# Kernel tuning notes

Measured on AMD Instinct MI355X. Metric: run time of the kernel, lower is better.

Reference implementation:

```python
import jax, jax.numpy as jnp
import numpy as np

NU, NI, DU, DI, E, B, T = 100000, 50000, 256, 256, 128, 8192, 24

def setup_inputs() -> dict:
    key = jax.random.key(0)
    ks = jax.random.split(key, 12)
    s = 0.05
    return {
        "nodes": jax.random.randint(ks[0], (B,), 0, NU),
        "neigh_idx": jax.random.randint(ks[1], (B, T), 0, NI),
        "u_weight": jax.random.normal(ks[2], (NU, DU), jnp.float32),
        "i_weight": jax.random.normal(ks[3], (NI, DI), jnp.float32),
        "uW": jax.random.normal(ks[4], (DU, E), jnp.float32) * s,
        "ub": jnp.zeros((E,), jnp.float32),
        "iW": jax.random.normal(ks[5], (DI, E), jnp.float32) * s,
        "ib": jnp.zeros((E,), jnp.float32),
        "aW1": jax.random.normal(ks[6], (2 * E, E), jnp.float32) * s,
        "ab1": jnp.zeros((E,), jnp.float32),
        "aW2": jax.random.normal(ks[7], (E, E), jnp.float32) * s,
        "ab2": jnp.zeros((E,), jnp.float32),
        "aW3": jax.random.normal(ks[8], (E, 1), jnp.float32) * s,
        "ab3": jnp.zeros((1,), jnp.float32),
    }


def reference(nodes, neigh_idx, u_weight, i_weight, uW, ub, iW, ib,
              aW1, ab1, aW2, ab2, aW3, ab3):
    # node features: u_layer(ufeature.weight[nodes])  -> [B, E]
    nodes_fea = u_weight[nodes] @ uW + ub
    # neighbor features: i_layer(ifeature.weight[interactions]) -> [B, T, E]
    neighs = i_weight[neigh_idx] @ iW + ib
    # attention MLP over cat(neigh_feat, node_feat.repeat) -> softmax over T
    x = jnp.concatenate(
        [neighs, jnp.broadcast_to(nodes_fea[:, None, :], neighs.shape)], axis=-1)
    h = jax.nn.relu(x @ aW1 + ab1)
    h = jax.nn.relu(h @ aW2 + ab2)
    logits = (h @ aW3 + ab3)[..., 0]            # [B, T]
    att = jax.nn.softmax(logits, axis=-1)       # softmax over neighbors (dim=0 per node)
    # attention-weighted aggregation: neighs_feature.T @ att_w  -> [B, E]
    agg = jnp.einsum('bt,bte->be', att, neighs)
    # scatter into embed_matrix rows of the batch nodes
    embed_matrix = jnp.zeros((NU, E), jnp.float32).at[nodes].set(agg)
    return nodes_fea, embed_matrix
```

## Files before the change

kernel.cpp:

```cpp
#include <hip/hip_runtime.h>
#include <math.h>

#define NU 100000
#define NI 50000
#define DK 256
#define EN 128
#define BB 8192
#define TT 24

typedef short short8 __attribute__((ext_vector_type(8)));
typedef float f32x4  __attribute__((ext_vector_type(4)));

#define WPACK_SHORTS 114688
#define WP_OFF     0
#define OWNER_OFF  229376
#define NTAB_OFF   629376
#define NPART_OFF  13429376

#define OFF_IWT   0
#define OFF_UWT   32768
#define OFF_AW1UT 65536
#define OFF_AW1LT 81920
#define OFF_AW2T  98304

#define NBLK_NEIGH 782
#define NBLK_NF    128
#define NBLK_PACK  448
#define ATTN_BLKS  (BB / 2)

__device__ __forceinline__ unsigned short f2b(float x) {
    unsigned int u = __float_as_uint(x);
    u = (u + 0x7FFFu + ((u >> 16) & 1u)) >> 16;
    return (unsigned short)u;
}
__device__ __forceinline__ float b2f(unsigned short v) {
    return __uint_as_float(((unsigned int)v) << 16);
}

#define MFMA(a, b, c) __builtin_amdgcn_mfma_f32_16x16x32_bf16((a), (b), (c), 0, 0, 0)
#define LDROW(buf, stride, row, k) \
    (*reinterpret_cast<const short8*>(reinterpret_cast<const char*>(buf) + (row) * (stride) + (k) * 2))

__global__ __launch_bounds__(256)
void prep_kernel(const int* __restrict__ nodes,
                 const float* __restrict__ uW, const float* __restrict__ iW,
                 const float* __restrict__ aW1, const float* __restrict__ aW2,
                 short* __restrict__ wp, int* __restrict__ owner)
{
    if (blockIdx.x < NBLK_PACK) {
        int i = blockIdx.x * 256 + threadIdx.x;
        float v;
        if (i < 32768)      { int j = i;         int n = j >> 8, k = j & 255; v = iW[k * EN + n]; }
        else if (i < 65536) { int j = i - 32768; int n = j >> 8, k = j & 255; v = uW[k * EN + n]; }
        else if (i < 81920) { int j = i - 65536; int n = j >> 7, k = j & 127; v = aW1[k * EN + n]; }
        else if (i < 98304) { int j = i - 81920; int n = j >> 7, k = j & 127; v = aW1[(128 + k) * EN + n]; }
        else                { int j = i - 98304; int n = j >> 7, k = j & 127; v = aW2[k * EN + n]; }
        wp[i] = (short)f2b(v);
    } else {
        int b = (blockIdx.x - NBLK_PACK) * 256 + threadIdx.x;
        if (b < BB) owner[nodes[b]] = -1;
    }
}

__global__ __launch_bounds__(256, 4)
void embed_kernel(const int* __restrict__ nodes,
                  const float* __restrict__ u_weight, const float* __restrict__ i_weight,
                  const float* __restrict__ ub, const float* __restrict__ ib,
                  const float* __restrict__ ab1,
                  const short* __restrict__ wp, int* __restrict__ owner,
                  short* __restrict__ ntab, float* __restrict__ out_nf,
                  float* __restrict__ npart)
{
    __shared__ __align__(16) char smem[33792];
    __shared__ int sNd[64];

    const int tid = threadIdx.x;
    const int l = tid & 63, lr = l & 15, lq = l >> 4, n0 = (tid >> 6) * 32;
    const int kA = lq * 8, nc0 = n0 + lr, nc1 = n0 + 16 + lr;

    if (blockIdx.x < NBLK_NEIGH) {
        const int r0 = blockIdx.x * 64;
        const int nrows = (NI - r0 < 64) ? (NI - r0) : 64;

        for (int task = tid; task < 64 * 32; task += 256) {
            int row = task >> 5, c = task & 31;
            if (row < nrows) {
                const float* src = i_weight + (size_t)(r0 + row) * DK + c * 8;
                float4 f0 = *(const float4*)src;
                float4 f1 = *(const float4*)(src + 4);
                short8 o;
                o[0]=f2b(f0.x); o[1]=f2b(f0.y); o[2]=f2b(f0.z); o[3]=f2b(f0.w);
                o[4]=f2b(f1.x); o[5]=f2b(f1.y); o[6]=f2b(f1.z); o[7]=f2b(f1.w);
                *reinterpret_cast<short8*>(smem + row * 528 + c * 16) = o;
            }
        }
        __syncthreads();

        const short* iWt = wp + OFF_IWT;
        f32x4 acc[4][2];
        #pragma unroll
        for (int m = 0; m < 4; ++m) { acc[m][0] = {0.f,0.f,0.f,0.f}; acc[m][1] = {0.f,0.f,0.f,0.f}; }
        #pragma unroll
        for (int ks = 0; ks < 8; ++ks) {
            int k = ks * 32 + kA;
            short8 w0 = *reinterpret_cast<const short8*>(iWt + nc0 * DK + k);
            short8 w1 = *reinterpret_cast<const short8*>(iWt + nc1 * DK + k);
            #pragma unroll
            for (int m = 0; m < 4; ++m) {
                short8 a = LDROW(smem, 528, m * 16 + lr, k);
                acc[m][0] = MFMA(a, w0, acc[m][0]);
                acc[m][1] = MFMA(a, w1, acc[m][1]);
            }
        }
        __syncthreads();
        {
            float ib0 = ib[nc0], ib1 = ib[nc1];
            #pragma unroll
            for (int m = 0; m < 4; ++m)
                #pragma unroll
                for (int nt = 0; nt < 2; ++nt) {
                    int n = nt ? nc1 : nc0;
                    float bv = nt ? ib1 : ib0;
                    #pragma unroll
                    for (int r = 0; r < 4; ++r) {
                        int row = m * 16 + lq * 4 + r;
                        *reinterpret_cast<short*>(smem + row * 264 + n * 2)
                            = (short)f2b(acc[m][nt][r] + bv);
                    }
                }
        }
        __syncthreads();
        for (int g = tid; g < nrows * 16; g += 256) {
            int row = g >> 4, s = g & 15;
            short8 v = *reinterpret_cast<const short8*>(smem + row * 264 + s * 16);
            *reinterpret_cast<short8*>(ntab + (size_t)(r0 + row) * EN + s * 8) = v;
        }
    } else {
        const int bblk = blockIdx.x - NBLK_NEIGH;
        const int r0 = bblk * 64;
        {
            int bq = bblk * 256 + tid;
            if (bq < BB) atomicMax(&owner[nodes[bq]], bq);
        }
        if (tid < 64) sNd[tid] = nodes[r0 + tid];
        __syncthreads();

        for (int task = tid; task < 64 * 32; task += 256) {
            int row = task >> 5, c = task & 31;
            const float* src = u_weight + (size_t)sNd[row] * DK + c * 8;
            float4 f0 = *(const float4*)src;
            float4 f1 = *(const float4*)(src + 4);
            short8 o;
            o[0]=f2b(f0.x); o[1]=f2b(f0.y); o[2]=f2b(f0.z); o[3]=f2b(f0.w);
            o[4]=f2b(f1.x); o[5]=f2b(f1.y); o[6]=f2b(f1.z); o[7]=f2b(f1.w);
            *reinterpret_cast<short8*>(smem + row * 528 + c * 16) = o;
        }
        __syncthreads();

        const short* uWt   = wp + OFF_UWT;
        const short* aW1Lt = wp + OFF_AW1LT;

        f32x4 acc[4][2];
        #pragma unroll
        for (int m = 0; m < 4; ++m) { acc[m][0] = {0.f,0.f,0.f,0.f}; acc[m][1] = {0.f,0.f,0.f,0.f}; }
        #pragma unroll
        for (int ks = 0; ks < 8; ++ks) {
            int k = ks * 32 + kA;
            short8 w0 = *reinterpret_cast<const short8*>(uWt + nc0 * DK + k);
            short8 w1 = *reinterpret_cast<const short8*>(uWt + nc1 * DK + k);
            #pragma unroll
            for (int m = 0; m < 4; ++m) {
                short8 a = LDROW(smem, 528, m * 16 + lr, k);
                acc[m][0] = MFMA(a, w0, acc[m][0]);
                acc[m][1] = MFMA(a, w1, acc[m][1]);
            }
        }
        __syncthreads();
        {
            float b0v = ub[nc0], b1v = ub[nc1];
            #pragma unroll
            for (int m = 0; m < 4; ++m)
                #pragma unroll
                for (int nt = 0; nt < 2; ++nt) {
                    int n = nt ? nc1 : nc0;
                    float bv = nt ? b1v : b0v;
                    #pragma unroll
                    for (int r = 0; r < 4; ++r) {
                        int row = m * 16 + lq * 4 + r;
                        float v = acc[m][nt][r] + bv;
                        out_nf[(size_t)(r0 + row) * EN + n] = v;
                        *reinterpret_cast<short*>(smem + row * 272 + n * 2) = (short)f2b(v);
                    }
                }
        }
        __syncthreads();

        f32x4 ap[4][2];
        #pragma unroll
        for (int m = 0; m < 4; ++m) { ap[m][0] = {0.f,0.f,0.f,0.f}; ap[m][1] = {0.f,0.f,0.f,0.f}; }
        #pragma unroll
        for (int ks = 0; ks < 4; ++ks) {
            int k = ks * 32 + kA;
            short8 w0 = *reinterpret_cast<const short8*>(aW1Lt + nc0 * EN + k);
            short8 w1 = *reinterpret_cast<const short8*>(aW1Lt + nc1 * EN + k);
            #pragma unroll
            for (int m = 0; m < 4; ++m) {
                short8 a = LDROW(smem, 272, m * 16 + lr, k);
                ap[m][0] = MFMA(a, w0, ap[m][0]);
                ap[m][1] = MFMA(a, w1, ap[m][1]);
            }
        }
        {
            float b0v = ab1[nc0], b1v = ab1[nc1];
            #pragma unroll
            for (int m = 0; m < 4; ++m)
                #pragma unroll
                for (int nt = 0; nt < 2; ++nt) {
                    int n = nt ? nc1 : nc0;
                    float bv = nt ? b1v : b0v;
                    #pragma unroll
                    for (int r = 0; r < 4; ++r) {
                        int row = m * 16 + lq * 4 + r;
                        npart[(size_t)(r0 + row) * EN + n] = ap[m][nt][r] + bv;
                    }
                }
        }
    }
}

__global__ __launch_bounds__(256, 4)
void attn_kernel(const int* __restrict__ nodes, const int* __restrict__ neigh_idx,
                 const float* __restrict__ ab2, const float* __restrict__ aW3,
                 const float* __restrict__ ab3, const short* __restrict__ wp,
                 const short* __restrict__ ntab, const float* __restrict__ npart,
                 const int* __restrict__ owner, float* __restrict__ out_embed)
{
    __shared__ __align__(16) short sNg[48 * 136];
    __shared__ __align__(16) short sH1[48 * 136];
    __shared__ float sNp[256];
    __shared__ float sLogP[4][48];
    __shared__ float sAtt[48];

    const int tid = threadIdx.x;
    const int b0  = blockIdx.x * 2;

    const int node0 = nodes[b0], node1 = nodes[b0 + 1];
    const int own0  = owner[node0], own1 = owner[node1];

    sNp[tid] = npart[(size_t)b0 * EN + tid];

    for (int task = tid; task < 48 * 16; task += 256) {
        int row = task >> 4, s = task & 15;
        int idx = neigh_idx[b0 * TT + row];
        short8 v = *reinterpret_cast<const short8*>(ntab + (size_t)idx * EN + s * 8);
        *reinterpret_cast<short8*>(reinterpret_cast<char*>(sNg) + row * 272 + s * 16) = v;
    }
    __syncthreads();

    const int l = tid & 63, lr = l & 15, lq = l >> 4;
    const int wid = tid >> 6, n0 = wid * 32;
    const int kA = lq * 8, nc0 = n0 + lr, nc1 = n0 + 16 + lr;
    const short* aW1Ut = wp + OFF_AW1UT;
    const short* aW2t  = wp + OFF_AW2T;

    f32x4 a1[3][2];
    #pragma unroll
    for (int m = 0; m < 3; ++m) { a1[m][0] = {0.f,0.f,0.f,0.f}; a1[m][1] = {0.f,0.f,0.f,0.f}; }
    #pragma unroll
    for (int ks = 0; ks < 4; ++ks) {
        int k = ks * 32 + kA;
        short8 w0 = *reinterpret_cast<const short8*>(aW1Ut + nc0 * EN + k);
        short8 w1 = *reinterpret_cast<const short8*>(aW1Ut + nc1 * EN + k);
        #pragma unroll
        for (int m = 0; m < 3; ++m) {
            short8 a = LDROW(sNg, 272, m * 16 + lr, k);
            a1[m][0] = MFMA(a, w0, a1[m][0]);
            a1[m][1] = MFMA(a, w1, a1[m][1]);
        }
    }
    #pragma unroll
    for (int m = 0; m < 3; ++m)
        #pragma unroll
        for (int nt = 0; nt < 2; ++nt) {
            int n = nt ? nc1 : nc0;
            #pragma unroll
            for (int r = 0; r < 4; ++r) {
                int row = m * 16 + lq * 4 + r;
                int g = (row >= TT) ? 1 : 0;
                float v = fmaxf(a1[m][nt][r] + sNp[g * EN + n], 0.f);
                *reinterpret_cast<short*>(reinterpret_cast<char*>(sH1) + row * 272 + n * 2)
                    = (short)f2b(v);
            }
        }
    __syncthreads();

    f32x4 a2[3][2];
    #pragma unroll
    for (int m = 0; m < 3; ++m) { a2[m][0] = {0.f,0.f,0.f,0.f}; a2[m][1] = {0.f,0.f,0.f,0.f}; }
    #pragma unroll
    for (int ks = 0; ks < 4; ++ks) {
        int k = ks * 32 + kA;
        short8 w0 = *reinterpret_cast<const short8*>(aW2t + nc0 * EN + k);
        short8 w1 = *reinterpret_cast<const short8*>(aW2t + nc1 * EN + k);
        #pragma unroll
        for (int m = 0; m < 3; ++m) {
            short8 a = LDROW(sH1, 272, m * 16 + lr, k);
            a2[m][0] = MFMA(a, w0, a2[m][0]);
            a2[m][1] = MFMA(a, w1, a2[m][1]);
        }
    }
    {
        float b0v = ab2[nc0], b1v = ab2[nc1];
        float w3a = aW3[nc0], w3b = aW3[nc1];
        #pragma unroll
        for (int m = 0; m < 3; ++m) {
            float lp[4];
            #pragma unroll
            for (int r = 0; r < 4; ++r) {
                float v0 = fmaxf(a2[m][0][r] + b0v, 0.f);
                float v1 = fmaxf(a2[m][1][r] + b1v, 0.f);
                lp[r] = v0 * w3a + v1 * w3b;
            }
            #pragma unroll
            for (int r = 0; r < 4; ++r) {
                float v = lp[r];
                v += __shfl_xor(v, 1, 16);
                v += __shfl_xor(v, 2, 16);
                v += __shfl_xor(v, 4, 16);
                v += __shfl_xor(v, 8, 16);
                if (lr == 0) sLogP[wid][m * 16 + lq * 4 + r] = v;
            }
        }
    }
    __syncthreads();

    if (tid < 64) {
        float s48 = 0.f;
        if (tid < 48)
            s48 = sLogP[0][tid] + sLogP[1][tid] + sLogP[2][tid] + sLogP[3][tid] + ab3[0];
        int g = tid >> 5, tt = tid & 31;
        float v = __shfl(s48, g * 24 + tt, 64);
        v = (tt < TT) ? v : -1e30f;
        float mx = v;
        #pragma unroll
        for (int d = 16; d > 0; d >>= 1) mx = fmaxf(mx, __shfl_xor(mx, d, 32));
        float p = (tt < TT) ? __expf(v - mx) : 0.f;
        float s = p;
        #pragma unroll
        for (int d = 16; d > 0; d >>= 1) s += __shfl_xor(s, d, 32);
        if (tt < TT) sAtt[g * TT + tt] = p / s;
    }
    __syncthreads();

    {
        int g = tid >> 7, e = tid & 127;
        float a = 0.f;
        #pragma unroll
        for (int t = 0; t < TT; ++t) {
            unsigned short nv = *reinterpret_cast<const unsigned short*>(
                reinterpret_cast<const char*>(sNg) + (g * TT + t) * 272 + e * 2);
            a += sAtt[g * TT + t] * b2f(nv);
        }
        int node = g ? node1 : node0;
        int own  = g ? own1  : own0;
        if (own == b0 + g)
            out_embed[(size_t)node * EN + e] = a;
    }

    {
        float4* embed4 = (float4*)out_embed;
        const int n16 = NU * EN / 4;
        const int gsz = ATTN_BLKS * 256;
        float4 z = {0.f, 0.f, 0.f, 0.f};
        for (int i = blockIdx.x * 256 + tid; i < n16; i += gsz) {
            if (owner[i >> 5] < 0) embed4[i] = z;
        }
    }
}

extern "C" void kernel_launch(void* const* d_in, const int* in_sizes, int n_in,
                              void* d_out, int out_size, void* d_ws, size_t ws_size,
                              hipStream_t stream) {
    const int*   nodes     = (const int*)d_in[0];
    const int*   neigh_idx = (const int*)d_in[1];
    const float* u_weight  = (const float*)d_in[2];
    const float* i_weight  = (const float*)d_in[3];
    const float* uW  = (const float*)d_in[4];
    const float* ub  = (const float*)d_in[5];
    const float* iW  = (const float*)d_in[6];
    const float* ib  = (const float*)d_in[7];
    const float* aW1 = (const float*)d_in[8];
    const float* ab1 = (const float*)d_in[9];
    const float* aW2 = (const float*)d_in[10];
    const float* ab2 = (const float*)d_in[11];
    const float* aW3 = (const float*)d_in[12];
    const float* ab3 = (const float*)d_in[13];

    float* out_nf    = (float*)d_out;
    float* out_embed = out_nf + (size_t)BB * EN;

    char*  ws    = (char*)d_ws;
    short* wpack = (short*)(ws + WP_OFF);
    int*   owner = (int*)(ws + OWNER_OFF);
    short* ntab  = (short*)(ws + NTAB_OFF);
    float* npart = (float*)(ws + NPART_OFF);

    prep_kernel<<<NBLK_PACK + 32, 256, 0, stream>>>(nodes, uW, iW, aW1, aW2, wpack, owner);
    embed_kernel<<<NBLK_NEIGH + NBLK_NF, 256, 0, stream>>>(
        nodes, u_weight, i_weight, ub, ib, ab1, wpack, owner, ntab, out_nf, npart);
    attn_kernel<<<ATTN_BLKS, 256, 0, stream>>>(nodes, neigh_idx, ab2, aW3, ab3,
                                               wpack, ntab, npart, owner, out_embed);
}
```

Before: 87.72 us.

## Process four nodes per attention block and move embed zero-fill into embed kernel

```diff
diff --git a/kernel.cpp b/kernel.cpp
--- a/kernel.cpp
+++ b/kernel.cpp
@@ -26,7 +26,8 @@
 #define NBLK_NEIGH 782
 #define NBLK_NF    128
 #define NBLK_PACK  448
-#define ATTN_BLKS  (BB / 2)
+#define GGA 4
+#define ATTN_BLKS  (BB / GGA)
 
 __device__ __forceinline__ unsigned short f2b(float x) {
     unsigned int u = __float_as_uint(x);
@@ -35,6 +36,11 @@
 }
 __device__ __forceinline__ float b2f(unsigned short v) {
     return __uint_as_float(((unsigned int)v) << 16);
+}
+__device__ __forceinline__ unsigned int cvtpk_bf16(float lo, float hi) {
+    unsigned int r;
+    asm("v_cvt_pk_bf16_f32 %0, %1, %2" : "=v"(r) : "v"(lo), "v"(hi));
+    return r;
 }
 
 #define MFMA(a, b, c) __builtin_amdgcn_mfma_f32_16x16x32_bf16((a), (b), (c), 0, 0, 0)
@@ -69,7 +75,7 @@
                   const float* __restrict__ ab1,
                   const short* __restrict__ wp, int* __restrict__ owner,
                   short* __restrict__ ntab, float* __restrict__ out_nf,
-                  float* __restrict__ npart)
+                  float* __restrict__ npart, float* __restrict__ out_embed)
 {
     __shared__ __align__(16) char smem[33792];
     __shared__ int sNd[64];
@@ -226,99 +232,113 @@
                 }
         }
     }
-}
-
-__global__ __launch_bounds__(256, 4)
+
+    {
+        float4* embed4 = (float4*)out_embed;
+        const int n16 = NU * EN / 4;
+        const int gsz = (NBLK_NEIGH + NBLK_NF) * 256;
+        float4 z = {0.f, 0.f, 0.f, 0.f};
+        for (int i = blockIdx.x * 256 + tid; i < n16; i += gsz) embed4[i] = z;
+    }
+}
+
+__global__ __launch_bounds__(256, 2)
 void attn_kernel(const int* __restrict__ nodes, const int* __restrict__ neigh_idx,
                  const float* __restrict__ ab2, const float* __restrict__ aW3,
                  const float* __restrict__ ab3, const short* __restrict__ wp,
                  const short* __restrict__ ntab, const float* __restrict__ npart,
                  const int* __restrict__ owner, float* __restrict__ out_embed)
 {
-    __shared__ __align__(16) short sNg[48 * 136];
-    __shared__ __align__(16) short sH1[48 * 136];
-    __shared__ float sNp[256];
-    __shared__ float sLogP[4][48];
-    __shared__ float sAtt[48];
+    __shared__ __align__(16) short sNg[96 * 136];
+    __shared__ __align__(16) short sH1[96 * 136];
+    __shared__ float sNpF[512];
+    __shared__ float sLogP[4][96];
 
     const int tid = threadIdx.x;
-    const int b0  = blockIdx.x * 2;
-
-    const int node0 = nodes[b0], node1 = nodes[b0 + 1];
-    const int own0  = owner[node0], own1 = owner[node1];
-
-    sNp[tid] = npart[(size_t)b0 * EN + tid];
-
-    for (int task = tid; task < 48 * 16; task += 256) {
-        int row = task >> 4, s = task & 15;
-        int idx = neigh_idx[b0 * TT + row];
+    const int b0  = blockIdx.x * GGA;
+    const int l   = tid & 63, w = tid >> 6;
+    const int lr  = l & 15, lq = l >> 4;
+    const int n0  = w * 32;
+    const int kA  = lq * 8, nc0 = n0 + lr, nc1 = n0 + 16 + lr;
+
+    sNpF[tid]       = npart[(size_t)b0 * EN + tid];
+    sNpF[tid + 256] = npart[(size_t)b0 * EN + 256 + tid];
+
+    #pragma unroll
+    for (int j = 0; j < 6; ++j) {
+        int task = j * 64 + l;
+        int trow = task >> 4, s = task & 15;
+        int idx = neigh_idx[(b0 + w) * TT + trow];
         short8 v = *reinterpret_cast<const short8*>(ntab + (size_t)idx * EN + s * 8);
-        *reinterpret_cast<short8*>(reinterpret_cast<char*>(sNg) + row * 272 + s * 16) = v;
+        *reinterpret_cast<short8*>(reinterpret_cast<char*>(sNg) + (w * 24 + trow) * 272 + s * 16) = v;
     }
     __syncthreads();
 
-    const int l = tid & 63, lr = l & 15, lq = l >> 4;
-    const int wid = tid >> 6, n0 = wid * 32;
-    const int kA = lq * 8, nc0 = n0 + lr, nc1 = n0 + 16 + lr;
     const short* aW1Ut = wp + OFF_AW1UT;
     const short* aW2t  = wp + OFF_AW2T;
 
-    f32x4 a1[3][2];
-    #pragma unroll
-    for (int m = 0; m < 3; ++m) { a1[m][0] = {0.f,0.f,0.f,0.f}; a1[m][1] = {0.f,0.f,0.f,0.f}; }
+    f32x4 acc[6][2];
+    #pragma unroll
+    for (int m = 0; m < 6; ++m) { acc[m][0] = {0.f,0.f,0.f,0.f}; acc[m][1] = {0.f,0.f,0.f,0.f}; }
     #pragma unroll
     for (int ks = 0; ks < 4; ++ks) {
         int k = ks * 32 + kA;
         short8 w0 = *reinterpret_cast<const short8*>(aW1Ut + nc0 * EN + k);
         short8 w1 = *reinterpret_cast<const short8*>(aW1Ut + nc1 * EN + k);
         #pragma unroll
-        for (int m = 0; m < 3; ++m) {
+        for (int m = 0; m < 6; ++m) {
             short8 a = LDROW(sNg, 272, m * 16 + lr, k);
-            a1[m][0] = MFMA(a, w0, a1[m][0]);
-            a1[m][1] = MFMA(a, w1, a1[m][1]);
-        }
-    }
-    #pragma unroll
-    for (int m = 0; m < 3; ++m)
+            acc[m][0] = MFMA(a, w0, acc[m][0]);
+            acc[m][1] = MFMA(a, w1, acc[m][1]);
+        }
+    }
+    #pragma unroll
+    for (int m = 0; m < 6; ++m) {
+        int g = (m == 0) ? 0 : (m == 1) ? ((lq < 2) ? 0 : 1)
+              : (m == 2) ? 1 : (m == 3) ? 2 : (m == 4) ? ((lq < 2) ? 2 : 3) : 3;
         #pragma unroll
         for (int nt = 0; nt < 2; ++nt) {
             int n = nt ? nc1 : nc0;
-            #pragma unroll
-            for (int r = 0; r < 4; ++r) {
-                int row = m * 16 + lq * 4 + r;
-                int g = (row >= TT) ? 1 : 0;
-                float v = fmaxf(a1[m][nt][r] + sNp[g * EN + n], 0.f);
-                *reinterpret_cast<short*>(reinterpret_cast<char*>(sH1) + row * 272 + n * 2)
-                    = (short)f2b(v);
-            }
-        }
+            float np = sNpF[g * EN + n];
+            float v0 = fmaxf(acc[m][nt][0] + np, 0.f);
+            float v1 = fmaxf(acc[m][nt][1] + np, 0.f);
+            float v2 = fmaxf(acc[m][nt][2] + np, 0.f);
+            float v3 = fmaxf(acc[m][nt][3] + np, 0.f);
+            unsigned int p01 = cvtpk_bf16(v0, v1);
+            unsigned int p23 = cvtpk_bf16(v2, v3);
+            char* base = reinterpret_cast<char*>(sH1) + (m * 16 + lq * 4) * 272 + n * 2;
+            *reinterpret_cast<short*>(base)       = (short)(p01 & 0xFFFF);
+            *reinterpret_cast<short*>(base + 272) = (short)(p01 >> 16);
+            *reinterpret_cast<short*>(base + 544) = (short)(p23 & 0xFFFF);
+            *reinterpret_cast<short*>(base + 816) = (short)(p23 >> 16);
+        }
+    }
     __syncthreads();
 
-    f32x4 a2[3][2];
-    #pragma unroll
-    for (int m = 0; m < 3; ++m) { a2[m][0] = {0.f,0.f,0.f,0.f}; a2[m][1] = {0.f,0.f,0.f,0.f}; }
+    #pragma unroll
+    for (int m = 0; m < 6; ++m) { acc[m][0] = {0.f,0.f,0.f,0.f}; acc[m][1] = {0.f,0.f,0.f,0.f}; }
     #pragma unroll
     for (int ks = 0; ks < 4; ++ks) {
         int k = ks * 32 + kA;
         short8 w0 = *reinterpret_cast<const short8*>(aW2t + nc0 * EN + k);
         short8 w1 = *reinterpret_cast<const short8*>(aW2t + nc1 * EN + k);
         #pragma unroll
-        for (int m = 0; m < 3; ++m) {
+        for (int m = 0; m < 6; ++m) {
             short8 a = LDROW(sH1, 272, m * 16 + lr, k);
-            a2[m][0] = MFMA(a, w0, a2[m][0]);
-            a2[m][1] = MFMA(a, w1, a2[m][1]);
+            acc[m][0] = MFMA(a, w0, acc[m][0]);
+            acc[m][1] = MFMA(a, w1, acc[m][1]);
         }
     }
     {
         float b0v = ab2[nc0], b1v = ab2[nc1];
         float w3a = aW3[nc0], w3b = aW3[nc1];
         #pragma unroll
-        for (int m = 0; m < 3; ++m) {
+        for (int m = 0; m < 6; ++m) {
             float lp[4];
             #pragma unroll
             for (int r = 0; r < 4; ++r) {
-                float v0 = fmaxf(a2[m][0][r] + b0v, 0.f);
-                float v1 = fmaxf(a2[m][1][r] + b1v, 0.f);
+                float v0 = fmaxf(acc[m][0][r] + b0v, 0.f);
+                float v1 = fmaxf(acc[m][1][r] + b1v, 0.f);
                 lp[r] = v0 * w3a + v1 * w3b;
             }
             #pragma unroll
@@ -328,52 +348,38 @@
                 v += __shfl_xor(v, 2, 16);
                 v += __shfl_xor(v, 4, 16);
                 v += __shfl_xor(v, 8, 16);
-                if (lr == 0) sLogP[wid][m * 16 + lq * 4 + r] = v;
+                if (lr == 0) sLogP[w][m * 16 + lq * 4 + r] = v;
             }
         }
     }
     __syncthreads();
 
-    if (tid < 64) {
-        float s48 = 0.f;
-        if (tid < 48)
-            s48 = sLogP[0][tid] + sLogP[1][tid] + sLogP[2][tid] + sLogP[3][tid] + ab3[0];
-        int g = tid >> 5, tt = tid & 31;
-        float v = __shfl(s48, g * 24 + tt, 64);
-        v = (tt < TT) ? v : -1e30f;
-        float mx = v;
-        #pragma unroll
-        for (int d = 16; d > 0; d >>= 1) mx = fmaxf(mx, __shfl_xor(mx, d, 32));
-        float p = (tt < TT) ? __expf(v - mx) : 0.f;
-        float s = p;
-        #pragma unroll
-        for (int d = 16; d > 0; d >>= 1) s += __shfl_xor(s, d, 32);
-        if (tt < TT) sAtt[g * TT + tt] = p / s;
-    }
-    __syncthreads();
+    float lg = -1e30f;
+    if (l < TT)
+        lg = sLogP[0][w * 24 + l] + sLogP[1][w * 24 + l]
+           + sLogP[2][w * 24 + l] + sLogP[3][w * 24 + l] + ab3[0];
+    float mx = lg;
+    #pragma unroll
+    for (int d = 32; d > 0; d >>= 1) mx = fmaxf(mx, __shfl_xor(mx, d, 64));
+    float p = (l < TT) ? __expf(lg - mx) : 0.f;
+    float s = p;
+    #pragma unroll
+    for (int d = 32; d > 0; d >>= 1) s += __shfl_xor(s, d, 64);
+    float att = p / s;
 
     {
-        int g = tid >> 7, e = tid & 127;
-        float a = 0.f;
+        float a0 = 0.f, a1 = 0.f;
         #pragma unroll
         for (int t = 0; t < TT; ++t) {
-            unsigned short nv = *reinterpret_cast<const unsigned short*>(
-                reinterpret_cast<const char*>(sNg) + (g * TT + t) * 272 + e * 2);
-            a += sAtt[g * TT + t] * b2f(nv);
-        }
-        int node = g ? node1 : node0;
-        int own  = g ? own1  : own0;
-        if (own == b0 + g)
-            out_embed[(size_t)node * EN + e] = a;
-    }
-
-    {
-        float4* embed4 = (float4*)out_embed;
-        const int n16 = NU * EN / 4;
-        const int gsz = ATTN_BLKS * 256;
-        float4 z = {0.f, 0.f, 0.f, 0.f};
-        for (int i = blockIdx.x * 256 + tid; i < n16; i += gsz) {
-            if (owner[i >> 5] < 0) embed4[i] = z;
+            float wt = __shfl(att, t, 64);
+            const char* rbase = reinterpret_cast<const char*>(sNg) + (w * 24 + t) * 272;
+            a0 += wt * b2f(*reinterpret_cast<const unsigned short*>(rbase + l * 2));
+            a1 += wt * b2f(*reinterpret_cast<const unsigned short*>(rbase + (l + 64) * 2));
+        }
+        int node = nodes[b0 + w];
+        if (owner[node] == b0 + w) {
+            out_embed[(size_t)node * EN + l]      = a0;
+            out_embed[(size_t)node * EN + 64 + l] = a1;
         }
     }
 }
@@ -407,7 +413,7 @@
 
     prep_kernel<<<NBLK_PACK + 32, 256, 0, stream>>>(nodes, uW, iW, aW1, aW2, wpack, owner);
     embed_kernel<<<NBLK_NEIGH + NBLK_NF, 256, 0, stream>>>(
-        nodes, u_weight, i_weight, ub, ib, ab1, wpack, owner, ntab, out_nf, npart);
+        nodes, u_weight, i_weight, ub, ib, ab1, wpack, owner, ntab, out_nf, npart, out_embed);
     attn_kernel<<<ATTN_BLKS, 256, 0, stream>>>(nodes, neigh_idx, ab2, aW3, ab3,
                                                wpack, ntab, npart, owner, out_embed);
 }
```

After: 79.78 us. -9.0%, faster.
